# Kernel tuning notes

Measured on AMD Instinct MI355X. Metric: run time of the kernel, lower is better.

Reference implementation:

```python
import jax, jax.numpy as jnp
import numpy as np

K = 5  # filter_size (matches init_kwargs)


def _adaptive_pool_matrix(size: int, k: int) -> jnp.ndarray:
    """Row-stochastic [k, size] matrix replicating torch adaptive_avg_pool1d bins."""
    P = np.zeros((k, size), np.float32)
    for i in range(k):
        s = (i * size) // k
        e = -((-(i + 1) * size) // k)  # ceil((i+1)*size/k)
        P[i, s:e] = 1.0 / (e - s)
    return jnp.asarray(P)


def setup_inputs() -> dict:
    key = jax.random.key(0)
    k1, k2, k3 = jax.random.split(key, 3)
    B, Cin, Cout, H, W = 8, 32, 32, 256, 256
    x = jax.random.normal(k1, (B, Cin, H, W), jnp.float32)
    conv_w = jax.random.normal(k2, (Cout, Cin), jnp.float32) * (1.0 / np.sqrt(Cin))
    conv_b = jax.random.normal(k3, (Cout,), jnp.float32) * 0.01
    return {"x": x, "conv_w": conv_w, "conv_b": conv_b}


def reference(x, conv_w, conv_b):
    B, Cin, H, W = x.shape
    # 1x1 conv == channel-mixing einsum
    feat = jnp.einsum('bihw,oi->bohw', x, conv_w) + conv_b[None, :, None, None]
    C = feat.shape[1]
    # adaptive_avg_pool2d(feat, K) via static pooling matrices -> per-(b,c) KxK filter
    Ph = _adaptive_pool_matrix(H, K)
    Pw = _adaptive_pool_matrix(W, K)
    filt = jnp.einsum('kh,bchw,lw->bckl', Ph, feat, Pw)  # [B, C, K, K]
    # pad per original intent ('same' output), then grouped conv with groups=B*C
    pad = (K - 1) // 2
    if (K - 1) % 2 == 0:
        p = ((pad, pad), (pad, pad))
    else:
        p = ((pad + 1, pad), (pad + 1, pad))
    inp = feat.reshape(1, B * C, H, W)
    w = filt.reshape(B * C, 1, K, K)
    out = jax.lax.conv_general_dilated(
        inp, w, window_strides=(1, 1), padding=p,
        dimension_numbers=('NCHW', 'OIHW', 'NCHW'),
        feature_group_count=B * C)
    return out.reshape(B, C, H, W)
```

## Files before the change

### kernel.cpp

```cpp
#include <hip/hip_runtime.h>


#define CIN 32
#define COUT 32
#define HW 256
#define PLANE (HW * HW)
#define BATCH 8
#define KF 5
#define BIN 52

__global__ __launch_bounds__(256) void pool_x_kernel(const float* __restrict__ x,
                                                     float* __restrict__ xpool) {
    int blk   = blockIdx.x;
    int s     = blk & 7;
    int plane = blk >> 3;
    int t     = threadIdx.x;
    int gy0   = s * 32;

    const float* xp = x + (size_t)plane * PLANE + (size_t)gy0 * HW + t;
    float acc[KF] = {0.f, 0.f, 0.f, 0.f, 0.f};
#pragma unroll
    for (int r = 0; r < 32; ++r) {
        float v  = xp[(size_t)r * HW];
        int   gy = gy0 + r;
#pragma unroll
        for (int k = 0; k < KF; ++k) {
            const int sk = (k * HW) / KF;
            if (gy >= sk && gy < sk + BIN) acc[k] += v;
        }
    }

    __shared__ float lds[KF][HW + 1];
#pragma unroll
    for (int k = 0; k < KF; ++k) lds[k][t] = acc[k];
    __syncthreads();

    if (t < KF * KF) {
        int kk = t / KF, ll = t - kk * KF;
        int sl = (ll * HW) / KF;
        float ssum = 0.f;
#pragma unroll 4
        for (int w = 0; w < BIN; ++w) ssum += lds[kk][sl + w];
        atomicAdd(&xpool[plane * 25 + t], ssum);
    }
}

__global__ __launch_bounds__(256) void conv_kernel(const float* __restrict__ x,
                                                   const float* __restrict__ Wm,
                                                   const float* __restrict__ bias,
                                                   float* __restrict__ feat) {
    int blk = blockIdx.x;
    int b   = blk >> 7;
    int rp  = blk & 127;
    int t   = threadIdx.x;
    int row = rp * 2 + (t >> 7);
    int c2  = (t & 127) * 2;

    const float* xb = x + (size_t)b * CIN * PLANE + (size_t)row * HW + c2;

    float a0[COUT], a1[COUT];
#pragma unroll
    for (int o = 0; o < COUT; ++o) { float bv = bias[o]; a0[o] = bv; a1[o] = bv; }

#pragma unroll
    for (int i = 0; i < CIN; ++i) {
        float2 xv = *(const float2*)(xb + (size_t)i * PLANE);
#pragma unroll
        for (int o = 0; o < COUT; ++o) {
            float w = Wm[o * CIN + i];
            a0[o] += w * xv.x;
            a1[o] += w * xv.y;
        }
    }

    float* fb = feat + (size_t)b * COUT * PLANE + (size_t)row * HW + c2;
#pragma unroll
    for (int o = 0; o < COUT; ++o) {
        float2 v; v.x = a0[o]; v.y = a1[o];
        *(float2*)(fb + (size_t)o * PLANE) = v;
    }
}

#define LROW 264
__global__ __launch_bounds__(256) void dwconv_kernel(const float* __restrict__ feat,
                                                     const float* __restrict__ xpool,
                                                     const float* __restrict__ Wm,
                                                     const float* __restrict__ bias,
                                                     float* __restrict__ out) {
    int bo    = blockIdx.y;
    int b     = bo >> 5;
    int o     = bo & 31;
    int strip = blockIdx.x;
    int gy0   = strip * 32;
    int t     = threadIdx.x;

    __shared__ __align__(16) float s[36 * LROW];
    __shared__ float sfilt[25];

    if (t < 25) {
        float acc = bias[o] * 2704.0f;
        const float* xp = xpool + (size_t)b * CIN * 25 + t;
#pragma unroll
        for (int i = 0; i < CIN; ++i) acc += Wm[o * CIN + i] * xp[i * 25];
        sfilt[t] = acc * (1.0f / 2704.0f);
    }
    if (t < 144) {
        int lr = t >> 2, e = t & 3;
        int ci = (e < 2) ? (2 + e) : (258 + e);
        s[lr * LROW + ci] = 0.f;
    }

    const float* fb = feat + (size_t)bo * PLANE;
#pragma unroll
    for (int j = 0; j < 9; ++j) {
        int idx = t + 256 * j;
        int lr  = idx >> 6;
        int cx  = (idx & 63) * 4;
        int gy  = gy0 - 2 + lr;
        float4 v = {0.f, 0.f, 0.f, 0.f};
        if ((unsigned)gy < (unsigned)HW) v = *(const float4*)(fb + (size_t)gy * HW + cx);
        *(float4*)(&s[lr * LROW + 4 + cx]) = v;
    }
    __syncthreads();

    float fw[25];
#pragma unroll
    for (int j = 0; j < 25; ++j) fw[j] = sfilt[j];

    int c = t;
    float w0[5], w1[5], w2[5], w3[5], w4[5];
#pragma unroll
    for (int j = 0; j < 5; ++j) {
        w0[j] = s[0 * LROW + 2 + c + j];
        w1[j] = s[1 * LROW + 2 + c + j];
        w2[j] = s[2 * LROW + 2 + c + j];
        w3[j] = s[3 * LROW + 2 + c + j];
    }
    float* ob = out + (size_t)bo * PLANE + (size_t)gy0 * HW + c;
#pragma unroll
    for (int r = 0; r < 32; ++r) {
#pragma unroll
        for (int j = 0; j < 5; ++j) w4[j] = s[(r + 4) * LROW + 2 + c + j];
        float acc = 0.f;
#pragma unroll
        for (int j = 0; j < 5; ++j) {
            acc += fw[0 * 5 + j] * w0[j];
            acc += fw[1 * 5 + j] * w1[j];
            acc += fw[2 * 5 + j] * w2[j];
            acc += fw[3 * 5 + j] * w3[j];
            acc += fw[4 * 5 + j] * w4[j];
        }
        ob[(size_t)r * HW] = acc;
#pragma unroll
        for (int j = 0; j < 5; ++j) {
            w0[j] = w1[j]; w1[j] = w2[j]; w2[j] = w3[j]; w3[j] = w4[j];
        }
    }
}

extern "C" void kernel_launch(void* const* d_in, const int* in_sizes, int n_in,
                              void* d_out, int out_size, void* d_ws, size_t ws_size,
                              hipStream_t stream) {
    const float* x      = (const float*)d_in[0];
    const float* conv_w = (const float*)d_in[1];
    const float* conv_b = (const float*)d_in[2];
    float* out = (float*)d_out;

    float* feat  = (float*)d_ws;
    float* xpool = feat + (size_t)BATCH * COUT * PLANE;

    hipMemsetAsync(xpool, 0, BATCH * CIN * 25 * sizeof(float), stream);
    pool_x_kernel<<<dim3(2048), dim3(256), 0, stream>>>(x, xpool);
    conv_kernel<<<dim3(1024), dim3(256), 0, stream>>>(x, conv_w, conv_b, feat);
    dwconv_kernel<<<dim3(8, BATCH * COUT), dim3(256), 0, stream>>>(feat, xpool, conv_w, conv_b, out);
}
```

Before: 189.7 us.

## Restructure 1x1 conv to one row per block and halve dwconv strip height

The 1x1 conv kernel now has each thread load all 32 input channels for one pixel into registers and compute the 32 outputs one at a time, instead of keeping 64 accumulators for two pixels. This lowers register pressure and raises occupancy, and the grid doubles to one row per block. The depthwise conv uses 16-row strips with a launch-bounds occupancy hint, which doubles the block count and shrinks the LDS footprint at the cost of more halo reloads. The conv launch is also moved ahead of the pooling kernel, so x may still be in cache when pooling reads it.

Result: faster. 165.4 us (-12.8%).

```diff
diff --git a/kernel.cpp b/kernel.cpp
--- a/kernel.cpp
+++ b/kernel.cpp
@@ -8,6 +8,30 @@
 #define BATCH 8
 #define KF 5
 #define BIN 52
+
+__global__ __launch_bounds__(256) void conv_kernel(const float* __restrict__ x,
+                                                   const float* __restrict__ Wm,
+                                                   const float* __restrict__ bias,
+                                                   float* __restrict__ feat) {
+    int blk = blockIdx.x;
+    int b   = blk >> 8;
+    int row = blk & 255;
+    int t   = threadIdx.x;
+
+    const float* xb = x + (size_t)b * CIN * PLANE + (size_t)row * HW + t;
+    float xv[CIN];
+#pragma unroll
+    for (int i = 0; i < CIN; ++i) xv[i] = xb[(size_t)i * PLANE];
+
+    float* fb = feat + (size_t)b * COUT * PLANE + (size_t)row * HW + t;
+#pragma unroll
+    for (int o = 0; o < COUT; ++o) {
+        float acc = bias[o];
+#pragma unroll
+        for (int i = 0; i < CIN; ++i) acc += Wm[o * CIN + i] * xv[i];
+        fb[(size_t)o * PLANE] = acc;
+    }
+}
 
 __global__ __launch_bounds__(256) void pool_x_kernel(const float* __restrict__ x,
                                                      float* __restrict__ xpool) {
@@ -45,56 +69,21 @@
     }
 }
 
-__global__ __launch_bounds__(256) void conv_kernel(const float* __restrict__ x,
-                                                   const float* __restrict__ Wm,
-                                                   const float* __restrict__ bias,
-                                                   float* __restrict__ feat) {
-    int blk = blockIdx.x;
-    int b   = blk >> 7;
-    int rp  = blk & 127;
-    int t   = threadIdx.x;
-    int row = rp * 2 + (t >> 7);
-    int c2  = (t & 127) * 2;
-
-    const float* xb = x + (size_t)b * CIN * PLANE + (size_t)row * HW + c2;
-
-    float a0[COUT], a1[COUT];
-#pragma unroll
-    for (int o = 0; o < COUT; ++o) { float bv = bias[o]; a0[o] = bv; a1[o] = bv; }
-
-#pragma unroll
-    for (int i = 0; i < CIN; ++i) {
-        float2 xv = *(const float2*)(xb + (size_t)i * PLANE);
-#pragma unroll
-        for (int o = 0; o < COUT; ++o) {
-            float w = Wm[o * CIN + i];
-            a0[o] += w * xv.x;
-            a1[o] += w * xv.y;
-        }
-    }
-
-    float* fb = feat + (size_t)b * COUT * PLANE + (size_t)row * HW + c2;
-#pragma unroll
-    for (int o = 0; o < COUT; ++o) {
-        float2 v; v.x = a0[o]; v.y = a1[o];
-        *(float2*)(fb + (size_t)o * PLANE) = v;
-    }
-}
-
+#define RS 16
 #define LROW 264
-__global__ __launch_bounds__(256) void dwconv_kernel(const float* __restrict__ feat,
-                                                     const float* __restrict__ xpool,
-                                                     const float* __restrict__ Wm,
-                                                     const float* __restrict__ bias,
-                                                     float* __restrict__ out) {
+__global__ __launch_bounds__(256, 6) void dwconv_kernel(const float* __restrict__ feat,
+                                                        const float* __restrict__ xpool,
+                                                        const float* __restrict__ Wm,
+                                                        const float* __restrict__ bias,
+                                                        float* __restrict__ out) {
     int bo    = blockIdx.y;
     int b     = bo >> 5;
     int o     = bo & 31;
     int strip = blockIdx.x;
-    int gy0   = strip * 32;
+    int gy0   = strip * RS;
     int t     = threadIdx.x;
 
-    __shared__ __align__(16) float s[36 * LROW];
+    __shared__ __align__(16) float s[(RS + 4) * LROW];
     __shared__ float sfilt[25];
 
     if (t < 25) {
@@ -104,7 +93,7 @@
         for (int i = 0; i < CIN; ++i) acc += Wm[o * CIN + i] * xp[i * 25];
         sfilt[t] = acc * (1.0f / 2704.0f);
     }
-    if (t < 144) {
+    if (t < (RS + 4) * 4) {
         int lr = t >> 2, e = t & 3;
         int ci = (e < 2) ? (2 + e) : (258 + e);
         s[lr * LROW + ci] = 0.f;
@@ -112,7 +101,7 @@
 
     const float* fb = feat + (size_t)bo * PLANE;
 #pragma unroll
-    for (int j = 0; j < 9; ++j) {
+    for (int j = 0; j < 5; ++j) {
         int idx = t + 256 * j;
         int lr  = idx >> 6;
         int cx  = (idx & 63) * 4;
@@ -138,7 +127,7 @@
     }
     float* ob = out + (size_t)bo * PLANE + (size_t)gy0 * HW + c;
 #pragma unroll
-    for (int r = 0; r < 32; ++r) {
+    for (int r = 0; r < RS; ++r) {
 #pragma unroll
         for (int j = 0; j < 5; ++j) w4[j] = s[(r + 4) * LROW + 2 + c + j];
         float acc = 0.f;
@@ -170,7 +159,7 @@
     float* xpool = feat + (size_t)BATCH * COUT * PLANE;
 
     hipMemsetAsync(xpool, 0, BATCH * CIN * 25 * sizeof(float), stream);
+    conv_kernel<<<dim3(BATCH * 256), dim3(256), 0, stream>>>(x, conv_w, conv_b, feat);
     pool_x_kernel<<<dim3(2048), dim3(256), 0, stream>>>(x, xpool);
-    conv_kernel<<<dim3(1024), dim3(256), 0, stream>>>(x, conv_w, conv_b, feat);
-    dwconv_kernel<<<dim3(8, BATCH * COUT), dim3(256), 0, stream>>>(feat, xpool, conv_w, conv_b, out);
+    dwconv_kernel<<<dim3(HW / RS, BATCH * COUT), dim3(256), 0, stream>>>(feat, xpool, conv_w, conv_b, out);
 }
```
